# Kernel tuning notes

Measured on AMD Instinct MI355X. Metric: run time of the kernel, lower is better.

The kernel has to match this reference:

```python
import jax, jax.numpy as jnp
import numpy as np

N = 100000        # nodes
E = 1600000       # directed edges (avg degree 16)
EMB = 32          # emb_hidden_dim
HID = 16          # hidden
Q = 0.25          # magnetic charge
NUM_SYMP = 15
BY = 4            # num_birthyear_disc


def _norm(edge_index, edge_weight):
    # Magnetic Laplacian, 'sym' normalization, lambda_max=2:
    # L_hat(u,v) = -deg^{-1/2}(u) * A_sym(u,v) * deg^{-1/2}(v) * exp(i*theta(u,v)),
    # theta = 2*pi*q*(A - A^T); diagonal of scaled L_hat is 0.
    src, dst = edge_index[0], edge_index[1]
    src2 = jnp.concatenate([src, dst])
    dst2 = jnp.concatenate([dst, src])
    sym_w = jnp.concatenate([edge_weight, edge_weight]) * 0.5
    theta = (2.0 * jnp.pi * Q) * jnp.concatenate([edge_weight, -edge_weight])
    deg = jax.ops.segment_sum(sym_w, dst2, num_segments=N)
    dinv = jnp.where(deg > 0, jax.lax.rsqrt(jnp.where(deg > 0, deg, 1.0)), 0.0)
    norm = dinv[src2] * sym_w * dinv[dst2]
    return src2, dst2, -norm * jnp.cos(theta), -norm * jnp.sin(theta)


def _cmatvec(src2, dst2, a_re, a_im, xr, xi):
    # complex sparse matvec: (A_re + i A_im)(x_re + i x_im)
    xr_s, xi_s = xr[src2], xi[src2]
    yr = jax.ops.segment_sum(a_re[:, None] * xr_s - a_im[:, None] * xi_s, dst2, num_segments=N)
    yi = jax.ops.segment_sum(a_re[:, None] * xi_s + a_im[:, None] * xr_s, dst2, num_segments=N)
    return yr, yi


def _magnet_conv(xr, xi, adj, W, b):
    # Chebyshev recursion T0=x, T1=L_hat x, T2=2 L_hat T1 - T0; out = sum_k T_k @ W[k] + b
    src2, dst2, a_re, a_im = adj
    out_r = xr @ W[0]
    out_i = xi @ W[0]
    t1r, t1i = _cmatvec(src2, dst2, a_re, a_im, xr, xi)
    out_r = out_r + t1r @ W[1]
    out_i = out_i + t1i @ W[1]
    t2r, t2i = _cmatvec(src2, dst2, a_re, a_im, t1r, t1i)
    t2r = 2.0 * t2r - xr
    t2i = 2.0 * t2i - xi
    out_r = out_r + t2r @ W[2]
    out_i = out_i + t2i @ W[2]
    return out_r + b, out_i + b


def setup_inputs() -> dict:
    key = jax.random.key(0)
    ks = jax.random.split(key, 12)
    birth = jax.random.randint(ks[0], (N,), 0, BY)
    gender = jax.random.randint(ks[1], (N,), 0, 2)
    symp = jax.random.randint(ks[2], (N, NUM_SYMP), 0, 3)
    x = jnp.concatenate([
        jax.nn.one_hot(birth, BY, dtype=jnp.int32),
        gender[:, None].astype(jnp.int32),
        symp.astype(jnp.int32),
    ], axis=1)  # [N, 20]
    edge_index = jax.random.randint(ks[3], (2, E), 0, N)
    edge_weight = jnp.ones((E,), jnp.float32)
    s = 0.1
    return {
        'x': x,
        'edge_index': edge_index,
        'edge_weight': edge_weight,
        'birth_tab': jax.random.normal(ks[4], (BY, EMB), jnp.float32) * s,
        'gender_tab': jax.random.normal(ks[5], (2, EMB), jnp.float32) * s,
        'symp_tab': jax.random.normal(ks[6], (NUM_SYMP, 3, EMB), jnp.float32) * s,
        'W1': jax.random.normal(ks[7], (3, EMB, HID), jnp.float32) * s,
        'b1': jnp.zeros((HID,), jnp.float32),
        'W2': jax.random.normal(ks[8], (3, HID, HID), jnp.float32) * s,
        'b2': jnp.zeros((HID,), jnp.float32),
        'Wc': jax.random.normal(ks[9], (2 * HID, 2 * HID), jnp.float32) * s,  # Conv1d k=1 (out,in)
        'bc': jnp.zeros((2 * HID,), jnp.float32),
        'Wl': jax.random.normal(ks[10], (2 * HID, 1), jnp.float32) * s,
        'bl': jnp.zeros((1,), jnp.float32),
    }


def reference(x, edge_index, edge_weight, birth_tab, gender_tab, symp_tab,
              W1, b1, W2, b2, Wc, bc, Wl, bl):
    # embedding gathers + mean fusion
    birth_idx = jnp.argmax(x[:, :BY] == 1, axis=1)
    birth_e = birth_tab[birth_idx]                              # [N, EMB]
    gender_e = gender_tab[x[:, BY]]                             # [N, EMB]
    symp_e = symp_tab[jnp.arange(NUM_SYMP)[None, :], x[:, -NUM_SYMP:]]  # [N, 15, EMB]
    feat = jnp.mean(symp_e, axis=1)
    h = (birth_e + gender_e + feat) / 3.0                       # [N, EMB]
    # complex Chebyshev spectral graph conv layers
    adj = _norm(edge_index, edge_weight)
    re, im = _magnet_conv(h, h, adj, W1, b1)
    re, im = _magnet_conv(re, im, adj, W2, b2)
    z = jnp.concatenate([re, im], axis=-1)                      # [N, 2*HID]
    z = z @ Wc.T + bc                                           # Conv1d kernel_size=1
    y = z @ Wl + bl                                             # Linear(2*HID, 1)
    return y[:, 0]
```

## Files before the change

kernel.cpp:

```cpp
#include <hip/hip_runtime.h>
#include <hip/hip_fp16.h>
#include <math.h>

static constexpr float PI2Q = 1.57079632679489662f;
#define NRANGE 8
#define NS2 16
#define GSH2 13
#define NKEY (NRANGE * NS2)
#define MAXRNG 13056

__device__ __forceinline__ float2 h2f_bits(int b) {
  __half2 h = *reinterpret_cast<__half2*>(&b);
  return __half22float2(h);
}
__device__ __forceinline__ int f2h_bits(float a, float b) {
  __half2 h = __floats2half2_rn(a, b);
  return *reinterpret_cast<int*>(&h);
}
__device__ __forceinline__ int grp_of(int s) {
  int g = s >> GSH2;
  return (g > NS2 - 1) ? (NS2 - 1) : g;
}

__global__ void k_weff(const float* __restrict__ Wc, const float* __restrict__ bc,
                       const float* __restrict__ Wl, const float* __restrict__ bl,
                       float* __restrict__ weff) {
  int k = threadIdx.x;
  if (k < 32) {
    float s = 0.f;
    #pragma unroll
    for (int j = 0; j < 32; ++j) s += Wc[j * 32 + k] * Wl[j];
    weff[k] = s;
  } else if (k == 32) {
    float s = 0.f;
    for (int j = 0; j < 32; ++j) s += bc[j] * Wl[j];
    weff[32] = s + bl[0];
  }
}

__global__ __launch_bounds__(256) void k_embed(
    const int* __restrict__ x, const float* __restrict__ btab,
    const float* __restrict__ gtab, const float* __restrict__ stab,
    const float* __restrict__ W1, const float* __restrict__ b1,
    float* __restrict__ PQ, __half2* __restrict__ PQh, float* __restrict__ o0, int n) {
  __shared__ float sm[3184];
  int tid = threadIdx.x;
  for (int t = tid; t < 1536; t += 256) sm[t] = W1[t];
  if (tid < 16) sm[1536 + tid] = b1[tid];
  for (int t = tid; t < 128; t += 256) sm[1552 + t] = btab[t];
  for (int t = tid; t < 64; t += 256) sm[1680 + t] = gtab[t];
  for (int t = tid; t < 1440; t += 256) sm[1744 + t] = stab[t];
  __syncthreads();
  int i = blockIdx.x * 256 + tid;
  if (i >= n) return;
  int xr[20];
  #pragma unroll
  for (int j = 0; j < 20; ++j) xr[j] = x[i * 20 + j];
  int bi = 0;
  #pragma unroll
  for (int j = 3; j >= 0; --j) if (xr[j] == 1) bi = j;
  int g = xr[4];
  float h[32];
  #pragma unroll
  for (int f = 0; f < 32; ++f) {
    float s = 0.f;
    #pragma unroll
    for (int j = 0; j < 15; ++j) s += sm[1744 + j * 96 + xr[5 + j] * 32 + f];
    h[f] = (sm[1552 + bi * 32 + f] + sm[1680 + g * 32 + f] + s * (1.f / 15.f)) * (1.f / 3.f);
  }
  #pragma unroll
  for (int f = 0; f < 16; ++f) {
    float o = sm[1536 + f], p = 0.f, q = 0.f;
    #pragma unroll
    for (int k = 0; k < 32; ++k) {
      float hk = h[k];
      o = fmaf(hk, sm[k * 16 + f], o);
      p = fmaf(hk, sm[512 + k * 16 + f], p);
      q = fmaf(hk, sm[1024 + k * 16 + f], q);
    }
    o0[i * 16 + f] = o;
    PQ[i * 32 + 2 * f] = p;
    PQ[i * 32 + 2 * f + 1] = q;
    PQh[(size_t)i * 16 + f] = __floats2half2_rn(p, q);
  }
}

__global__ __launch_bounds__(256) void k_rhist(const int* __restrict__ ei, int* __restrict__ rcnt,
                                               int rng, int E_) {
  __shared__ int h[NKEY * 8];
  int tid = threadIdx.x;
  for (int t = tid; t < NKEY * 8; t += 256) h[t] = 0;
  __syncthreads();
  int slot = tid & 7;
  int stride = gridDim.x * 256;
  for (int e = blockIdx.x * 256 + tid; e < E_; e += stride) {
    int s = ei[e], d = ei[E_ + e];
    int keyA = ((d / rng) << 4) | grp_of(s);
    int keyB = ((s / rng) << 4) | grp_of(d);
    atomicAdd(&h[keyA * 8 + slot], 1);
    atomicAdd(&h[keyB * 8 + slot], 1);
  }
  __syncthreads();
  for (int t = tid; t < NKEY; t += 256) {
    int sum = 0;
    #pragma unroll
    for (int j = 0; j < 8; ++j) sum += h[t * 8 + j];
    if (sum) atomicAdd(&rcnt[t], sum);
  }
}

__global__ void k_rbase(const int* __restrict__ rcnt, int* __restrict__ rbase, int* __restrict__ rcur) {
  if (threadIdx.x == 0) {
    int run = 0;
    for (int r = 0; r < NKEY; ++r) { rbase[r] = run; rcur[r] = run; run += rcnt[r]; }
    rbase[NKEY] = run;
  }
}

__global__ __launch_bounds__(256) void k_bucket(const int* __restrict__ ei, const float* __restrict__ ew,
                                                int* __restrict__ rcur, int* __restrict__ brow,
                                                int2* __restrict__ bsw, int rng, int E_) {
  __shared__ int lcnt[NKEY];
  __shared__ int gbase[NKEY];
  int tid = threadIdx.x;
  if (tid < NKEY) lcnt[tid] = 0;
  __syncthreads();
  int e0 = blockIdx.x * 1024;
  int s[4], d[4], wb[4], kA[4], kB[4], la[4], lb[4];
  #pragma unroll
  for (int j = 0; j < 4; ++j) {
    int e = e0 + j * 256 + tid;
    if (e < E_) {
      s[j] = ei[e]; d[j] = ei[E_ + e]; wb[j] = __float_as_int(ew[e]);
      kA[j] = ((d[j] / rng) << 4) | grp_of(s[j]);
      kB[j] = ((s[j] / rng) << 4) | grp_of(d[j]);
      la[j] = atomicAdd(&lcnt[kA[j]], 1);
      lb[j] = atomicAdd(&lcnt[kB[j]], 1);
    } else {
      kA[j] = -1; kB[j] = -1; s[j] = 0; d[j] = 0; wb[j] = 0; la[j] = 0; lb[j] = 0;
    }
  }
  __syncthreads();
  if (tid < NKEY) gbase[tid] = lcnt[tid] ? atomicAdd(&rcur[tid], lcnt[tid]) : 0;
  __syncthreads();
  #pragma unroll
  for (int j = 0; j < 4; ++j) {
    if (kA[j] >= 0) {
      int pA = gbase[kA[j]] + la[j];
      brow[pA] = d[j];
      bsw[pA] = make_int2(s[j], wb[j]);
      int pB = gbase[kB[j]] + lb[j];
      brow[pB] = s[j];
      bsw[pB] = make_int2(d[j] | (int)0x80000000, wb[j]);
    }
  }
}

__global__ __launch_bounds__(1024) void k_hist2(const int* __restrict__ brow, const int* __restrict__ rbase,
                                                int* __restrict__ Hg, int rng) {
  __shared__ int hist[MAXRNG];
  int r = blockIdx.x & (NRANGE - 1);
  int st = blockIdx.x >> 3;
  int key = (r << 4) | st;
  int tid = threadIdx.x;
  for (int t = tid; t < rng; t += 1024) hist[t] = 0;
  __syncthreads();
  int k0 = rbase[key], k1 = rbase[key + 1];
  int base = r * rng;
  for (int k = k0 + tid; k < k1; k += 1024)
    atomicAdd(&hist[brow[k] - base], 1);
  __syncthreads();
  int* plane = Hg + (size_t)(r * NS2 + st) * rng;
  for (int t = tid; t < rng; t += 1024) plane[t] = hist[t];
}

__global__ __launch_bounds__(512) void k_scanH(int* __restrict__ Hg, int* __restrict__ cnt,
                                               int rng, int n) {
  int v = blockIdx.x * 512 + threadIdx.x;
  if (v >= n) return;
  int r = v / rng;
  int vloc = v - r * rng;
  int run = 0;
  size_t idx = (size_t)(r * NS2) * rng + vloc;
  #pragma unroll 4
  for (int s = 0; s < NS2; ++s) {
    int t = Hg[idx];
    Hg[idx] = run;
    run += t;
    idx += rng;
  }
  cnt[v] = run;
}

__global__ __launch_bounds__(1024) void k_scan_a(const int* __restrict__ cnt, int* __restrict__ rowp,
                                                 int* __restrict__ bsum, int n) {
  __shared__ int sh[1024];
  int tid = threadIdx.x;
  int idx = blockIdx.x * 1024 + tid;
  int v = (idx < n) ? cnt[idx] : 0;
  sh[tid] = v;
  __syncthreads();
  for (int offd = 1; offd < 1024; offd <<= 1) {
    int t = (tid >= offd) ? sh[tid - offd] : 0;
    __syncthreads();
    sh[tid] += t;
    __syncthreads();
  }
  if (idx < n) rowp[idx] = sh[tid] - v;
  if (tid == 1023) bsum[blockIdx.x] = sh[1023];
}

__global__ __launch_bounds__(128) void k_scan_b(int* __restrict__ bsum, int nb,
                                                int* __restrict__ rowp, int n) {
  __shared__ int sh[128];
  int tid = threadIdx.x;
  int v = (tid < nb) ? bsum[tid] : 0;
  sh[tid] = v;
  __syncthreads();
  for (int offd = 1; offd < 128; offd <<= 1) {
    int t = (tid >= offd) ? sh[tid - offd] : 0;
    __syncthreads();
    sh[tid] += t;
    __syncthreads();
  }
  if (tid < nb) bsum[tid] = sh[tid] - v;
  if (tid == 127) rowp[n] = sh[127];
}

__global__ __launch_bounds__(1024) void k_scan_c(int* __restrict__ rowp, const int* __restrict__ bsum, int n) {
  int idx = blockIdx.x * 1024 + threadIdx.x;
  if (idx < n && blockIdx.x > 0) rowp[idx] += bsum[blockIdx.x];
}

__global__ __launch_bounds__(1024) void k_place2(const int* __restrict__ brow, const int2* __restrict__ bsw,
                                                 const int* __restrict__ rbase, const int* __restrict__ rowp,
                                                 const int* __restrict__ Hoff, int2* __restrict__ recs,
                                                 int rng) {
  __shared__ int hist[MAXRNG];
  int r = blockIdx.x & (NRANGE - 1);
  int st = blockIdx.x >> 3;
  int key = (r << 4) | st;
  int tid = threadIdx.x;
  for (int t = tid; t < rng; t += 1024) hist[t] = 0;
  __syncthreads();
  int k0 = rbase[key], k1 = rbase[key + 1];
  int base = r * rng;
  const int* plane = Hoff + (size_t)(r * NS2 + st) * rng;
  for (int k = k0 + tid; k < k1; k += 1024) {
    int row = brow[k];
    int rowloc = row - base;
    int lr = atomicAdd(&hist[rowloc], 1);
    recs[rowp[row] + plane[rowloc] + lr] = bsw[k];
  }
}

__global__ __launch_bounds__(256) void k_rowdeg(const int* __restrict__ rowp, const int2* __restrict__ recs,
                                                float* __restrict__ dinv, int n) {
  int wid = (blockIdx.x * 256 + threadIdx.x) >> 6;
  if (wid >= n) return;
  int lane = threadIdx.x & 63;
  int rs = rowp[wid], re = rowp[wid + 1];
  float sum = 0.f;
  for (int k = rs + lane; k < re; k += 64) sum += __int_as_float(recs[k].y);
  sum += __shfl_xor(sum, 1); sum += __shfl_xor(sum, 2);
  sum += __shfl_xor(sum, 4); sum += __shfl_xor(sum, 8);
  sum += __shfl_xor(sum, 16); sum += __shfl_xor(sum, 32);
  if (lane == 0) {
    float dg = 0.5f * sum;
    dinv[wid] = (dg > 0.f) ? rsqrtf(dg) : 0.f;
  }
}

__global__ __launch_bounds__(256) void k_norm(const int* __restrict__ rowp, int2* __restrict__ recs,
                                              const float* __restrict__ dinv, int n) {
  int wid = (blockIdx.x * 256 + threadIdx.x) >> 6;
  if (wid >= n) return;
  int lane = threadIdx.x & 63;
  float di = dinv[wid];
  int rs = rowp[wid], re = rowp[wid + 1];
  for (int k = rs + lane; k < re; k += 64) {
    int2 r = recs[k];
    int s = r.x & 0x7fffffff;
    float w = __int_as_float(r.y);
    float nrm = di * 0.5f * w * dinv[s];
    float sn, cs;
    sincosf(PI2Q * w, &sn, &cs);
    float ar = -nrm * cs;
    float ai = (r.x < 0) ? nrm * sn : -nrm * sn;
    recs[k].y = f2h_bits(ar, ai);
  }
}

__global__ __launch_bounds__(256, 8) void k_hop_sym(
    const int* __restrict__ rowp, const int2* __restrict__ recs,
    const __half2* __restrict__ PQh, __half2* __restrict__ Uh, float* __restrict__ AB, int n) {
  int wid = (blockIdx.x * 256 + threadIdx.x) >> 6;
  if (wid >= n) return;
  int lane = threadIdx.x & 63;
  int fq = lane & 3, su = lane >> 2;
  int rs = rowp[wid], rend = rowp[wid + 1];
  float aA[4] = {0.f, 0.f, 0.f, 0.f}, aB[4] = {0.f, 0.f, 0.f, 0.f};
  float aC[4] = {0.f, 0.f, 0.f, 0.f}, aD[4] = {0.f, 0.f, 0.f, 0.f};
  const long long* rq = reinterpret_cast<const long long*>(recs);
  const int4* Pq = reinterpret_cast<const int4*>(PQh);
  for (int k = rs + su; k < rend; k += 16) {
    long long r0 = __builtin_nontemporal_load(rq + k);
    int s = ((int)r0) & 0x7fffffff;
    float2 a = h2f_bits((int)(r0 >> 32));
    float wm = a.x - a.y, wp = a.x + a.y;
    int4 v = Pq[(size_t)s * 4 + fq];
    float2 x0 = h2f_bits(v.x), x1 = h2f_bits(v.y), x2 = h2f_bits(v.z), x3 = h2f_bits(v.w);
    aA[0] = fmaf(wm, x0.x, aA[0]); aB[0] = fmaf(wp, x0.x, aB[0]);
    aC[0] = fmaf(wm, x0.y, aC[0]); aD[0] = fmaf(wp, x0.y, aD[0]);
    aA[1] = fmaf(wm, x1.x, aA[1]); aB[1] = fmaf(wp, x1.x, aB[1]);
    aC[1] = fmaf(wm, x1.y, aC[1]); aD[1] = fmaf(wp, x1.y, aD[1]);
    aA[2] = fmaf(wm, x2.x, aA[2]); aB[2] = fmaf(wp, x2.x, aB[2]);
    aC[2] = fmaf(wm, x2.y, aC[2]); aD[2] = fmaf(wp, x2.y, aD[2]);
    aA[3] = fmaf(wm, x3.x, aA[3]); aB[3] = fmaf(wp, x3.x, aB[3]);
    aC[3] = fmaf(wm, x3.y, aC[3]); aD[3] = fmaf(wp, x3.y, aD[3]);
  }
  #pragma unroll
  for (int j = 0; j < 4; ++j) {
    aA[j] += __shfl_xor(aA[j], 4); aA[j] += __shfl_xor(aA[j], 8);
    aA[j] += __shfl_xor(aA[j], 16); aA[j] += __shfl_xor(aA[j], 32);
    aB[j] += __shfl_xor(aB[j], 4); aB[j] += __shfl_xor(aB[j], 8);
    aB[j] += __shfl_xor(aB[j], 16); aB[j] += __shfl_xor(aB[j], 32);
    aC[j] += __shfl_xor(aC[j], 4); aC[j] += __shfl_xor(aC[j], 8);
    aC[j] += __shfl_xor(aC[j], 16); aC[j] += __shfl_xor(aC[j], 32);
    aD[j] += __shfl_xor(aD[j], 4); aD[j] += __shfl_xor(aD[j], 8);
    aD[j] += __shfl_xor(aD[j], 16); aD[j] += __shfl_xor(aD[j], 32);
  }
  if (lane < 4) {
    *reinterpret_cast<float4*>(AB + wid * 32 + 8 * fq) = make_float4(aA[0], aB[0], aA[1], aB[1]);
    *reinterpret_cast<float4*>(AB + wid * 32 + 8 * fq + 4) = make_float4(aA[2], aB[2], aA[3], aB[3]);
    int4 hv;
    hv.x = f2h_bits(aC[0], aD[0]); hv.y = f2h_bits(aC[1], aD[1]);
    hv.z = f2h_bits(aC[2], aD[2]); hv.w = f2h_bits(aC[3], aD[3]);
    *reinterpret_cast<int4*>(Uh + (size_t)wid * 16 + 4 * fq) = hv;
  }
}

template <int MODE>
__global__ __launch_bounds__(256, 8) void k_hop_full(
    const int* __restrict__ rowp, const int2* __restrict__ recs,
    const __half2* __restrict__ Xh, float* __restrict__ Y, __half2* __restrict__ Yh,
    const float* __restrict__ o0, const float* __restrict__ AB, const float* __restrict__ PQ,
    const float* __restrict__ D, const float* __restrict__ weff, int n) {
  int wid = (blockIdx.x * 256 + threadIdx.x) >> 6;
  if (wid >= n) return;
  int lane = threadIdx.x & 63;
  int fq = lane & 3, su = lane >> 2;
  int rs = rowp[wid], rend = rowp[wid + 1];
  float aR[4] = {0.f, 0.f, 0.f, 0.f}, aI[4] = {0.f, 0.f, 0.f, 0.f};
  const long long* rq = reinterpret_cast<const long long*>(recs);
  const int4* Xq = reinterpret_cast<const int4*>(Xh);
  for (int k = rs + su; k < rend; k += 16) {
    long long r0 = __builtin_nontemporal_load(rq + k);
    int s = ((int)r0) & 0x7fffffff;
    float2 a = h2f_bits((int)(r0 >> 32));
    int4 v = Xq[(size_t)s * 4 + fq];
    float2 x0 = h2f_bits(v.x), x1 = h2f_bits(v.y), x2 = h2f_bits(v.z), x3 = h2f_bits(v.w);
    aR[0] = fmaf(a.x, x0.x, aR[0]); aR[0] = fmaf(-a.y, x0.y, aR[0]);
    aI[0] = fmaf(a.x, x0.y, aI[0]); aI[0] = fmaf(a.y, x0.x, aI[0]);
    aR[1] = fmaf(a.x, x1.x, aR[1]); aR[1] = fmaf(-a.y, x1.y, aR[1]);
    aI[1] = fmaf(a.x, x1.y, aI[1]); aI[1] = fmaf(a.y, x1.x, aI[1]);
    aR[2] = fmaf(a.x, x2.x, aR[2]); aR[2] = fmaf(-a.y, x2.y, aR[2]);
    aI[2] = fmaf(a.x, x2.y, aI[2]); aI[2] = fmaf(a.y, x2.x, aI[2]);
    aR[3] = fmaf(a.x, x3.x, aR[3]); aR[3] = fmaf(-a.y, x3.y, aR[3]);
    aI[3] = fmaf(a.x, x3.y, aI[3]); aI[3] = fmaf(a.y, x3.x, aI[3]);
  }
  #pragma unroll
  for (int j = 0; j < 4; ++j) {
    aR[j] += __shfl_xor(aR[j], 4); aR[j] += __shfl_xor(aR[j], 8);
    aR[j] += __shfl_xor(aR[j], 16); aR[j] += __shfl_xor(aR[j], 32);
    aI[j] += __shfl_xor(aI[j], 4); aI[j] += __shfl_xor(aI[j], 8);
    aI[j] += __shfl_xor(aI[j], 16); aI[j] += __shfl_xor(aI[j], 32);
  }
  if (MODE == 2) {
    float c = 0.f;
    if (lane < 4) {
      float4 d0 = *reinterpret_cast<const float4*>(D + wid * 32 + 8 * fq);
      float4 d1 = *reinterpret_cast<const float4*>(D + wid * 32 + 8 * fq + 4);
      float4 w0 = *reinterpret_cast<const float4*>(weff + 4 * fq);
      float4 w1 = *reinterpret_cast<const float4*>(weff + 16 + 4 * fq);
      c  = (d0.x + 2.f * aR[0]) * w0.x + (d0.y + 2.f * aI[0]) * w1.x;
      c += (d0.z + 2.f * aR[1]) * w0.y + (d0.w + 2.f * aI[1]) * w1.y;
      c += (d1.x + 2.f * aR[2]) * w0.z + (d1.y + 2.f * aI[2]) * w1.z;
      c += (d1.z + 2.f * aR[3]) * w0.w + (d1.w + 2.f * aI[3]) * w1.w;
    }
    c += __shfl_xor(c, 1); c += __shfl_xor(c, 2);
    if (lane == 0) Y[wid] = c + weff[32];
  } else if (lane < 4) {
    if (MODE == 0) {
      *reinterpret_cast<float4*>(Y + wid * 32 + 8 * fq) = make_float4(aR[0], aI[0], aR[1], aI[1]);
      *reinterpret_cast<float4*>(Y + wid * 32 + 8 * fq + 4) = make_float4(aR[2], aI[2], aR[3], aI[3]);
    } else {
      float4 o = *reinterpret_cast<const float4*>(o0 + wid * 16 + 4 * fq);
      float4 ab0 = *reinterpret_cast<const float4*>(AB + wid * 32 + 8 * fq);
      float4 ab1 = *reinterpret_cast<const float4*>(AB + wid * 32 + 8 * fq + 4);
      float4 pq0 = *reinterpret_cast<const float4*>(PQ + wid * 32 + 8 * fq);
      float4 pq1 = *reinterpret_cast<const float4*>(PQ + wid * 32 + 8 * fq + 4);
      float zr0 = o.x + ab0.x + 2.f * aR[0] - pq0.y;
      float zi0 = o.x + ab0.y + 2.f * aI[0] - pq0.y;
      float zr1 = o.y + ab0.z + 2.f * aR[1] - pq0.w;
      float zi1 = o.y + ab0.w + 2.f * aI[1] - pq0.w;
      float zr2 = o.z + ab1.x + 2.f * aR[2] - pq1.y;
      float zi2 = o.z + ab1.y + 2.f * aI[2] - pq1.y;
      float zr3 = o.w + ab1.z + 2.f * aR[3] - pq1.w;
      float zi3 = o.w + ab1.w + 2.f * aI[3] - pq1.w;
      *reinterpret_cast<float4*>(Y + wid * 32 + 8 * fq) = make_float4(zr0, zi0, zr1, zi1);
      *reinterpret_cast<float4*>(Y + wid * 32 + 8 * fq + 4) = make_float4(zr2, zi2, zr3, zi3);
      int4 hv;
      hv.x = f2h_bits(zr0, zi0); hv.y = f2h_bits(zr1, zi1);
      hv.z = f2h_bits(zr2, zi2); hv.w = f2h_bits(zr3, zi3);
      *reinterpret_cast<int4*>(Yh + (size_t)wid * 16 + 4 * fq) = hv;
    }
  }
}

__global__ __launch_bounds__(256) void k_d2(const float* __restrict__ X2, const float* __restrict__ T1,
                                            const float* __restrict__ W2g, const float* __restrict__ b2g,
                                            __half2* __restrict__ U2h, float* __restrict__ D, int n) {
  __shared__ float sm[1040];
  int tid = threadIdx.x;
  for (int t = tid; t < 768; t += 256) sm[t] = W2g[t];
  if (tid < 16) sm[768 + tid] = b2g[tid];
  __syncthreads();
  if (tid < 256) sm[784 + tid] = sm[tid] - sm[512 + tid];
  __syncthreads();
  int i = blockIdx.x * 256 + tid;
  if (i >= n) return;
  float re[16], im[16], tr[16], ti[16];
  #pragma unroll
  for (int k = 0; k < 16; ++k) {
    float2 a = *reinterpret_cast<const float2*>(X2 + i * 32 + 2 * k);
    re[k] = a.x; im[k] = a.y;
    float2 b = *reinterpret_cast<const float2*>(T1 + i * 32 + 2 * k);
    tr[k] = b.x; ti[k] = b.y;
  }
  #pragma unroll
  for (int f = 0; f < 16; ++f) {
    float ur = 0.f, ui = 0.f;
    float dr = sm[768 + f], di = sm[768 + f];
    #pragma unroll
    for (int k = 0; k < 16; ++k) {
      float w2 = sm[512 + k * 16 + f];
      float w1 = sm[256 + k * 16 + f];
      float w02 = sm[784 + k * 16 + f];
      ur = fmaf(tr[k], w2, ur);
      ui = fmaf(ti[k], w2, ui);
      dr = fmaf(re[k], w02, dr); dr = fmaf(tr[k], w1, dr);
      di = fmaf(im[k], w02, di); di = fmaf(ti[k], w1, di);
    }
    U2h[(size_t)i * 16 + f] = __floats2half2_rn(ur, ui);
    *reinterpret_cast<float2*>(D + i * 32 + 2 * f) = make_float2(dr, di);
  }
}

extern "C" void kernel_launch(void* const* d_in, const int* in_sizes, int n_in,
                              void* d_out, int out_size, void* d_ws, size_t ws_size,
                              hipStream_t stream) {
  const int* x = (const int*)d_in[0];
  const int* ei = (const int*)d_in[1];
  const float* ew = (const float*)d_in[2];
  const float* btab = (const float*)d_in[3];
  const float* gtab = (const float*)d_in[4];
  const float* stab = (const float*)d_in[5];
  const float* W1 = (const float*)d_in[6];
  const float* b1 = (const float*)d_in[7];
  const float* W2 = (const float*)d_in[8];
  const float* b2 = (const float*)d_in[9];
  const float* Wc = (const float*)d_in[10];
  const float* bc = (const float*)d_in[11];
  const float* Wl = (const float*)d_in[12];
  const float* bl = (const float*)d_in[13];
  float* yout = (float*)d_out;

  const int N_ = in_sizes[0] / 20;
  const int E_ = in_sizes[1] / 2;
  const int M_ = 2 * E_;
  const int rng = (N_ + NRANGE - 1) / NRANGE;

  size_t off = 0;
  auto take = [&](size_t bytes) -> void* {
    void* p = (char*)d_ws + off;
    off += (bytes + 255) & ~(size_t)255;
    return p;
  };
  float* PQ   = (float*)take((size_t)N_ * 32 * 4);
  float* o0   = (float*)take((size_t)N_ * 16 * 4);
  float* Ubuf = (float*)take((size_t)N_ * 32 * 4);
  float* ABuf = (float*)take((size_t)N_ * 32 * 4);
  float* X2   = (float*)take((size_t)N_ * 32 * 4);
  float* dinv = (float*)take((size_t)N_ * 4);
  int* cnt    = (int*)take((size_t)N_ * 4);
  int* rowp   = (int*)take((size_t)(N_ + 1) * 4);
  int* bsum   = (int*)take(1024 * 4);
  float* weff = (float*)take(64 * 4);
  int* rcnt   = (int*)take(NKEY * 4);
  int* rbase  = (int*)take((NKEY + 1) * 4);
  int* rcur   = (int*)take(NKEY * 4);
  int* brow   = (int*)take((size_t)M_ * 4);
  int2* bsw   = (int2*)take((size_t)M_ * 8);
  int2* recs  = (int2*)take((size_t)M_ * 8);
  (void)ws_size; (void)n_in; (void)out_size;

  int* Hg      = (int*)PQ;
  __half2* PQh = (__half2*)brow;
  __half2* Uh  = (__half2*)((char*)brow + (size_t)N_ * 64);
  __half2* X2h = (__half2*)bsw;
  __half2* U2h = (__half2*)((char*)bsw + (size_t)N_ * 64);

  int nbN = (N_ + 255) / 256;
  int nbS = (N_ + 1023) / 1024;
  int nbH = (N_ + 3) / 4;
  int nbT = (N_ + 511) / 512;
  int nbB = (E_ + 1023) / 1024;

  hipMemsetAsync(rcnt, 0, NKEY * 4, stream);

  k_weff<<<1, 64, 0, stream>>>(Wc, bc, Wl, bl, weff);

  k_rhist<<<512, 256, 0, stream>>>(ei, rcnt, rng, E_);
  k_rbase<<<1, 64, 0, stream>>>(rcnt, rbase, rcur);
  k_bucket<<<nbB, 256, 0, stream>>>(ei, ew, rcur, brow, bsw, rng, E_);
  k_hist2<<<NRANGE * NS2, 1024, 0, stream>>>(brow, rbase, Hg, rng);
  k_scanH<<<nbT, 512, 0, stream>>>(Hg, cnt, rng, N_);
  k_scan_a<<<nbS, 1024, 0, stream>>>(cnt, rowp, bsum, N_);
  k_scan_b<<<1, 128, 0, stream>>>(bsum, nbS, rowp, N_);
  k_scan_c<<<nbS, 1024, 0, stream>>>(rowp, bsum, N_);
  k_place2<<<NRANGE * NS2, 1024, 0, stream>>>(brow, bsw, rbase, rowp, Hg, recs, rng);

  k_embed<<<nbN, 256, 0, stream>>>(x, btab, gtab, stab, W1, b1, PQ, PQh, o0, N_);
  k_rowdeg<<<nbH, 256, 0, stream>>>(rowp, recs, dinv, N_);
  k_norm<<<nbH, 256, 0, stream>>>(rowp, recs, dinv, N_);

  k_hop_sym<<<nbH, 256, 0, stream>>>(rowp, recs, PQh, Uh, ABuf, N_);
  k_hop_full<1><<<nbH, 256, 0, stream>>>(rowp, recs, Uh, X2, X2h, o0, ABuf, PQ,
                                         nullptr, nullptr, N_);
  k_hop_full<0><<<nbH, 256, 0, stream>>>(rowp, recs, X2h, Ubuf, nullptr, nullptr,
                                         nullptr, nullptr, nullptr, nullptr, N_);
  k_d2<<<nbN, 256, 0, stream>>>(X2, Ubuf, W2, b2, U2h, ABuf, N_);
  k_hop_full<2><<<nbH, 256, 0, stream>>>(rowp, recs, U2h, yout, nullptr, nullptr,
                                         nullptr, nullptr, ABuf, weff, N_);
}
```

Before: 540.1 us.

## Build CSR via 512-row chunk buckets and fuse degree/normalization into placement

```diff
diff --git a/kernel.cpp b/kernel.cpp
--- a/kernel.cpp
+++ b/kernel.cpp
@@ -3,11 +3,9 @@
 #include <math.h>
 
 static constexpr float PI2Q = 1.57079632679489662f;
-#define NRANGE 8
-#define NS2 16
-#define GSH2 13
-#define NKEY (NRANGE * NS2)
-#define MAXRNG 13056
+#define CSH 9
+#define CROWS 512
+#define MAXKEY 256
 
 __device__ __forceinline__ float2 h2f_bits(int b) {
   __half2 h = *reinterpret_cast<__half2*>(&b);
@@ -16,10 +14,6 @@
 __device__ __forceinline__ int f2h_bits(float a, float b) {
   __half2 h = __floats2half2_rn(a, b);
   return *reinterpret_cast<int*>(&h);
-}
-__device__ __forceinline__ int grp_of(int s) {
-  int g = s >> GSH2;
-  return (g > NS2 - 1) ? (NS2 - 1) : g;
 }
 
 __global__ void k_weff(const float* __restrict__ Wc, const float* __restrict__ bc,
@@ -86,22 +80,20 @@
 }
 
 __global__ __launch_bounds__(256) void k_rhist(const int* __restrict__ ei, int* __restrict__ rcnt,
-                                               int rng, int E_) {
-  __shared__ int h[NKEY * 8];
-  int tid = threadIdx.x;
-  for (int t = tid; t < NKEY * 8; t += 256) h[t] = 0;
+                                               int E_) {
+  __shared__ int h[MAXKEY * 8];
+  int tid = threadIdx.x;
+  for (int t = tid; t < MAXKEY * 8; t += 256) h[t] = 0;
   __syncthreads();
   int slot = tid & 7;
   int stride = gridDim.x * 256;
   for (int e = blockIdx.x * 256 + tid; e < E_; e += stride) {
     int s = ei[e], d = ei[E_ + e];
-    int keyA = ((d / rng) << 4) | grp_of(s);
-    int keyB = ((s / rng) << 4) | grp_of(d);
-    atomicAdd(&h[keyA * 8 + slot], 1);
-    atomicAdd(&h[keyB * 8 + slot], 1);
-  }
-  __syncthreads();
-  for (int t = tid; t < NKEY; t += 256) {
+    atomicAdd(&h[(d >> CSH) * 8 + slot], 1);
+    atomicAdd(&h[(s >> CSH) * 8 + slot], 1);
+  }
+  __syncthreads();
+  for (int t = tid; t < MAXKEY; t += 256) {
     int sum = 0;
     #pragma unroll
     for (int j = 0; j < 8; ++j) sum += h[t * 8 + j];
@@ -109,31 +101,32 @@
   }
 }
 
-__global__ void k_rbase(const int* __restrict__ rcnt, int* __restrict__ rbase, int* __restrict__ rcur) {
+__global__ void k_rbase(const int* __restrict__ rcnt, int* __restrict__ rbase, int* __restrict__ rcur,
+                        int nkey) {
   if (threadIdx.x == 0) {
     int run = 0;
-    for (int r = 0; r < NKEY; ++r) { rbase[r] = run; rcur[r] = run; run += rcnt[r]; }
-    rbase[NKEY] = run;
+    for (int r = 0; r < nkey; ++r) { rbase[r] = run; rcur[r] = run; run += rcnt[r]; }
+    rbase[nkey] = run;
   }
 }
 
 __global__ __launch_bounds__(256) void k_bucket(const int* __restrict__ ei, const float* __restrict__ ew,
                                                 int* __restrict__ rcur, int* __restrict__ brow,
-                                                int2* __restrict__ bsw, int rng, int E_) {
-  __shared__ int lcnt[NKEY];
-  __shared__ int gbase[NKEY];
-  int tid = threadIdx.x;
-  if (tid < NKEY) lcnt[tid] = 0;
-  __syncthreads();
-  int e0 = blockIdx.x * 1024;
-  int s[4], d[4], wb[4], kA[4], kB[4], la[4], lb[4];
-  #pragma unroll
-  for (int j = 0; j < 4; ++j) {
+                                                int2* __restrict__ bsw, int E_) {
+  __shared__ int lcnt[MAXKEY];
+  __shared__ int gbase[MAXKEY];
+  int tid = threadIdx.x;
+  lcnt[tid] = 0;
+  __syncthreads();
+  int e0 = blockIdx.x * 2048;
+  int s[8], d[8], wb[8], kA[8], kB[8], la[8], lb[8];
+  #pragma unroll
+  for (int j = 0; j < 8; ++j) {
     int e = e0 + j * 256 + tid;
     if (e < E_) {
       s[j] = ei[e]; d[j] = ei[E_ + e]; wb[j] = __float_as_int(ew[e]);
-      kA[j] = ((d[j] / rng) << 4) | grp_of(s[j]);
-      kB[j] = ((s[j] / rng) << 4) | grp_of(d[j]);
+      kA[j] = d[j] >> CSH;
+      kB[j] = s[j] >> CSH;
       la[j] = atomicAdd(&lcnt[kA[j]], 1);
       lb[j] = atomicAdd(&lcnt[kB[j]], 1);
     } else {
@@ -141,10 +134,10 @@
     }
   }
   __syncthreads();
-  if (tid < NKEY) gbase[tid] = lcnt[tid] ? atomicAdd(&rcur[tid], lcnt[tid]) : 0;
-  __syncthreads();
-  #pragma unroll
-  for (int j = 0; j < 4; ++j) {
+  gbase[tid] = lcnt[tid] ? atomicAdd(&rcur[tid], lcnt[tid]) : 0;
+  __syncthreads();
+  #pragma unroll
+  for (int j = 0; j < 8; ++j) {
     if (kA[j] >= 0) {
       int pA = gbase[kA[j]] + la[j];
       brow[pA] = d[j];
@@ -156,138 +149,66 @@
   }
 }
 
-__global__ __launch_bounds__(1024) void k_hist2(const int* __restrict__ brow, const int* __restrict__ rbase,
-                                                int* __restrict__ Hg, int rng) {
-  __shared__ int hist[MAXRNG];
-  int r = blockIdx.x & (NRANGE - 1);
-  int st = blockIdx.x >> 3;
-  int key = (r << 4) | st;
-  int tid = threadIdx.x;
-  for (int t = tid; t < rng; t += 1024) hist[t] = 0;
-  __syncthreads();
-  int k0 = rbase[key], k1 = rbase[key + 1];
-  int base = r * rng;
-  for (int k = k0 + tid; k < k1; k += 1024)
-    atomicAdd(&hist[brow[k] - base], 1);
-  __syncthreads();
-  int* plane = Hg + (size_t)(r * NS2 + st) * rng;
-  for (int t = tid; t < rng; t += 1024) plane[t] = hist[t];
-}
-
-__global__ __launch_bounds__(512) void k_scanH(int* __restrict__ Hg, int* __restrict__ cnt,
-                                               int rng, int n) {
-  int v = blockIdx.x * 512 + threadIdx.x;
-  if (v >= n) return;
-  int r = v / rng;
-  int vloc = v - r * rng;
-  int run = 0;
-  size_t idx = (size_t)(r * NS2) * rng + vloc;
-  #pragma unroll 4
-  for (int s = 0; s < NS2; ++s) {
-    int t = Hg[idx];
-    Hg[idx] = run;
-    run += t;
-    idx += rng;
-  }
-  cnt[v] = run;
-}
-
-__global__ __launch_bounds__(1024) void k_scan_a(const int* __restrict__ cnt, int* __restrict__ rowp,
-                                                 int* __restrict__ bsum, int n) {
-  __shared__ int sh[1024];
-  int tid = threadIdx.x;
-  int idx = blockIdx.x * 1024 + tid;
-  int v = (idx < n) ? cnt[idx] : 0;
-  sh[tid] = v;
-  __syncthreads();
-  for (int offd = 1; offd < 1024; offd <<= 1) {
-    int t = (tid >= offd) ? sh[tid - offd] : 0;
+__global__ __launch_bounds__(1024) void k_chunkdeg(const int* __restrict__ brow, const int2* __restrict__ bsw,
+                                                   const int* __restrict__ rbase, int* __restrict__ rowp,
+                                                   float* __restrict__ dinv, int n, int nkey) {
+  __shared__ int hist[CROWS];
+  __shared__ float wsum[CROWS];
+  __shared__ int pref[CROWS];
+  int c = blockIdx.x;
+  int base = c << CSH;
+  int rows = min(CROWS, n - base);
+  int tid = threadIdx.x;
+  if (tid < CROWS) { hist[tid] = 0; wsum[tid] = 0.f; }
+  __syncthreads();
+  int k0 = rbase[c], k1 = rbase[c + 1];
+  for (int k = k0 + tid; k < k1; k += 1024) {
+    int rl = brow[k] - base;
+    atomicAdd(&hist[rl], 1);
+    atomicAdd(&wsum[rl], __int_as_float(bsw[k].y));
+  }
+  __syncthreads();
+  if (tid < CROWS) pref[tid] = hist[tid];
+  __syncthreads();
+  for (int off = 1; off < CROWS; off <<= 1) {
+    int t = (tid < CROWS && tid >= off) ? pref[tid - off] : 0;
     __syncthreads();
-    sh[tid] += t;
+    if (tid < CROWS) pref[tid] += t;
     __syncthreads();
   }
-  if (idx < n) rowp[idx] = sh[tid] - v;
-  if (tid == 1023) bsum[blockIdx.x] = sh[1023];
-}
-
-__global__ __launch_bounds__(128) void k_scan_b(int* __restrict__ bsum, int nb,
-                                                int* __restrict__ rowp, int n) {
-  __shared__ int sh[128];
-  int tid = threadIdx.x;
-  int v = (tid < nb) ? bsum[tid] : 0;
-  sh[tid] = v;
-  __syncthreads();
-  for (int offd = 1; offd < 128; offd <<= 1) {
-    int t = (tid >= offd) ? sh[tid - offd] : 0;
-    __syncthreads();
-    sh[tid] += t;
-    __syncthreads();
-  }
-  if (tid < nb) bsum[tid] = sh[tid] - v;
-  if (tid == 127) rowp[n] = sh[127];
-}
-
-__global__ __launch_bounds__(1024) void k_scan_c(int* __restrict__ rowp, const int* __restrict__ bsum, int n) {
-  int idx = blockIdx.x * 1024 + threadIdx.x;
-  if (idx < n && blockIdx.x > 0) rowp[idx] += bsum[blockIdx.x];
-}
-
-__global__ __launch_bounds__(1024) void k_place2(const int* __restrict__ brow, const int2* __restrict__ bsw,
-                                                 const int* __restrict__ rbase, const int* __restrict__ rowp,
-                                                 const int* __restrict__ Hoff, int2* __restrict__ recs,
-                                                 int rng) {
-  __shared__ int hist[MAXRNG];
-  int r = blockIdx.x & (NRANGE - 1);
-  int st = blockIdx.x >> 3;
-  int key = (r << 4) | st;
-  int tid = threadIdx.x;
-  for (int t = tid; t < rng; t += 1024) hist[t] = 0;
-  __syncthreads();
-  int k0 = rbase[key], k1 = rbase[key + 1];
-  int base = r * rng;
-  const int* plane = Hoff + (size_t)(r * NS2 + st) * rng;
+  if (tid < rows) {
+    rowp[base + tid] = k0 + pref[tid] - hist[tid];
+    float dg = 0.5f * wsum[tid];
+    dinv[base + tid] = (dg > 0.f) ? rsqrtf(dg) : 0.f;
+  }
+  if (c == 0 && tid == 0) rowp[n] = rbase[nkey];
+}
+
+__global__ __launch_bounds__(1024) void k_chunkplace(const int* __restrict__ brow, const int2* __restrict__ bsw,
+                                                     const int* __restrict__ rbase, const int* __restrict__ rowp,
+                                                     const float* __restrict__ dinv, int2* __restrict__ recs,
+                                                     int n) {
+  __shared__ int cur[CROWS];
+  __shared__ float dloc[CROWS];
+  int c = blockIdx.x;
+  int base = c << CSH;
+  int rows = min(CROWS, n - base);
+  int tid = threadIdx.x;
+  if (tid < rows) { cur[tid] = rowp[base + tid]; dloc[tid] = dinv[base + tid]; }
+  __syncthreads();
+  int k0 = rbase[c], k1 = rbase[c + 1];
   for (int k = k0 + tid; k < k1; k += 1024) {
-    int row = brow[k];
-    int rowloc = row - base;
-    int lr = atomicAdd(&hist[rowloc], 1);
-    recs[rowp[row] + plane[rowloc] + lr] = bsw[k];
-  }
-}
-
-__global__ __launch_bounds__(256) void k_rowdeg(const int* __restrict__ rowp, const int2* __restrict__ recs,
-                                                float* __restrict__ dinv, int n) {
-  int wid = (blockIdx.x * 256 + threadIdx.x) >> 6;
-  if (wid >= n) return;
-  int lane = threadIdx.x & 63;
-  int rs = rowp[wid], re = rowp[wid + 1];
-  float sum = 0.f;
-  for (int k = rs + lane; k < re; k += 64) sum += __int_as_float(recs[k].y);
-  sum += __shfl_xor(sum, 1); sum += __shfl_xor(sum, 2);
-  sum += __shfl_xor(sum, 4); sum += __shfl_xor(sum, 8);
-  sum += __shfl_xor(sum, 16); sum += __shfl_xor(sum, 32);
-  if (lane == 0) {
-    float dg = 0.5f * sum;
-    dinv[wid] = (dg > 0.f) ? rsqrtf(dg) : 0.f;
-  }
-}
-
-__global__ __launch_bounds__(256) void k_norm(const int* __restrict__ rowp, int2* __restrict__ recs,
-                                              const float* __restrict__ dinv, int n) {
-  int wid = (blockIdx.x * 256 + threadIdx.x) >> 6;
-  if (wid >= n) return;
-  int lane = threadIdx.x & 63;
-  float di = dinv[wid];
-  int rs = rowp[wid], re = rowp[wid + 1];
-  for (int k = rs + lane; k < re; k += 64) {
-    int2 r = recs[k];
-    int s = r.x & 0x7fffffff;
-    float w = __int_as_float(r.y);
-    float nrm = di * 0.5f * w * dinv[s];
+    int rl = brow[k] - base;
+    int2 p = bsw[k];
+    int s = p.x & 0x7fffffff;
+    float w = __int_as_float(p.y);
+    float nrm = dloc[rl] * 0.5f * w * dinv[s];
     float sn, cs;
     sincosf(PI2Q * w, &sn, &cs);
     float ar = -nrm * cs;
-    float ai = (r.x < 0) ? nrm * sn : -nrm * sn;
-    recs[k].y = f2h_bits(ar, ai);
+    float ai = (p.x < 0) ? nrm * sn : -nrm * sn;
+    int pos = atomicAdd(&cur[rl], 1);
+    recs[pos] = make_int2(p.x, f2h_bits(ar, ai));
   }
 }
 
@@ -479,7 +400,7 @@
   const int N_ = in_sizes[0] / 20;
   const int E_ = in_sizes[1] / 2;
   const int M_ = 2 * E_;
-  const int rng = (N_ + NRANGE - 1) / NRANGE;
+  const int nkey = (N_ + CROWS - 1) >> CSH;
 
   size_t off = 0;
   auto take = [&](size_t bytes) -> void* {
@@ -493,47 +414,36 @@
   float* ABuf = (float*)take((size_t)N_ * 32 * 4);
   float* X2   = (float*)take((size_t)N_ * 32 * 4);
   float* dinv = (float*)take((size_t)N_ * 4);
-  int* cnt    = (int*)take((size_t)N_ * 4);
   int* rowp   = (int*)take((size_t)(N_ + 1) * 4);
-  int* bsum   = (int*)take(1024 * 4);
   float* weff = (float*)take(64 * 4);
-  int* rcnt   = (int*)take(NKEY * 4);
-  int* rbase  = (int*)take((NKEY + 1) * 4);
-  int* rcur   = (int*)take(NKEY * 4);
+  int* rcnt   = (int*)take(MAXKEY * 4);
+  int* rbase  = (int*)take((MAXKEY + 1) * 4);
+  int* rcur   = (int*)take(MAXKEY * 4);
   int* brow   = (int*)take((size_t)M_ * 4);
   int2* bsw   = (int2*)take((size_t)M_ * 8);
   int2* recs  = (int2*)take((size_t)M_ * 8);
   (void)ws_size; (void)n_in; (void)out_size;
 
-  int* Hg      = (int*)PQ;
   __half2* PQh = (__half2*)brow;
   __half2* Uh  = (__half2*)((char*)brow + (size_t)N_ * 64);
   __half2* X2h = (__half2*)bsw;
   __half2* U2h = (__half2*)((char*)bsw + (size_t)N_ * 64);
 
   int nbN = (N_ + 255) / 256;
-  int nbS = (N_ + 1023) / 1024;
   int nbH = (N_ + 3) / 4;
-  int nbT = (N_ + 511) / 512;
-  int nbB = (E_ + 1023) / 1024;
-
-  hipMemsetAsync(rcnt, 0, NKEY * 4, stream);
+  int nbB = (E_ + 2047) / 2048;
+
+  hipMemsetAsync(rcnt, 0, MAXKEY * 4, stream);
 
   k_weff<<<1, 64, 0, stream>>>(Wc, bc, Wl, bl, weff);
 
-  k_rhist<<<512, 256, 0, stream>>>(ei, rcnt, rng, E_);
-  k_rbase<<<1, 64, 0, stream>>>(rcnt, rbase, rcur);
-  k_bucket<<<nbB, 256, 0, stream>>>(ei, ew, rcur, brow, bsw, rng, E_);
-  k_hist2<<<NRANGE * NS2, 1024, 0, stream>>>(brow, rbase, Hg, rng);
-  k_scanH<<<nbT, 512, 0, stream>>>(Hg, cnt, rng, N_);
-  k_scan_a<<<nbS, 1024, 0, stream>>>(cnt, rowp, bsum, N_);
-  k_scan_b<<<1, 128, 0, stream>>>(bsum, nbS, rowp, N_);
-  k_scan_c<<<nbS, 1024, 0, stream>>>(rowp, bsum, N_);
-  k_place2<<<NRANGE * NS2, 1024, 0, stream>>>(brow, bsw, rbase, rowp, Hg, recs, rng);
+  k_rhist<<<512, 256, 0, stream>>>(ei, rcnt, E_);
+  k_rbase<<<1, 64, 0, stream>>>(rcnt, rbase, rcur, nkey);
+  k_bucket<<<nbB, 256, 0, stream>>>(ei, ew, rcur, brow, bsw, E_);
+  k_chunkdeg<<<nkey, 1024, 0, stream>>>(brow, bsw, rbase, rowp, dinv, N_, nkey);
+  k_chunkplace<<<nkey, 1024, 0, stream>>>(brow, bsw, rbase, rowp, dinv, recs, N_);
 
   k_embed<<<nbN, 256, 0, stream>>>(x, btab, gtab, stab, W1, b1, PQ, PQh, o0, N_);
-  k_rowdeg<<<nbH, 256, 0, stream>>>(rowp, recs, dinv, N_);
-  k_norm<<<nbH, 256, 0, stream>>>(rowp, recs, dinv, N_);
 
   k_hop_sym<<<nbH, 256, 0, stream>>>(rowp, recs, PQh, Uh, ABuf, N_);
   k_hop_full<1><<<nbH, 256, 0, stream>>>(rowp, recs, Uh, X2, X2h, o0, ABuf, PQ,
```

Result: faster. 452.2 us (-16.3%).
